# Kernel tuning notes

Hardware: AMD Instinct MI355X
Metric: run time of the kernel (lower is better)

Reference implementation:

```python
import jax, jax.numpy as jnp
import numpy as np

N, M, D = 8192, 8192, 256

def setup_inputs() -> dict:
    key = jax.random.key(0)
    ks = jax.random.split(key, 8)
    s = 1.0 / np.sqrt(D)
    return {
        "x_q": jax.random.normal(ks[0], (N, D), dtype=jnp.float32),
        "x_kv": jax.random.normal(ks[1], (M, D), dtype=jnp.float32),
        "Wq": jax.random.uniform(ks[2], (D, D), minval=-s, maxval=s, dtype=jnp.float32),
        "bq": jax.random.uniform(ks[3], (D,), minval=-s, maxval=s, dtype=jnp.float32),
        "Wk": jax.random.uniform(ks[4], (D, D), minval=-s, maxval=s, dtype=jnp.float32),
        "bk": jax.random.uniform(ks[5], (D,), minval=-s, maxval=s, dtype=jnp.float32),
        "Wv": jax.random.uniform(ks[6], (D, D), minval=-s, maxval=s, dtype=jnp.float32),
        "bv": jax.random.uniform(ks[7], (D,), minval=-s, maxval=s, dtype=jnp.float32),
    }

def reference(x_q, x_kv, Wq, bq, Wk, bk, Wv, bv):
    # Linear layers: y = x @ W^T + b (torch convention: W is [out, in])
    q = x_q @ Wq.T + bq          # [N, D]
    k = x_kv @ Wk.T + bk         # [M, D]
    v = x_kv @ Wv.T + bv         # [M, D]
    scale = jnp.sqrt(jnp.asarray(q.shape[1], q.dtype))
    attn = jnp.einsum('nd,md->nm', q, k) / scale  # [N, M]
    attn = jax.nn.softmax(attn, axis=1)
    return attn @ v              # [N, D]
```

## Files before the change

### kernel.cpp

```cpp
#include <hip/hip_runtime.h>

#define NN 8192
#define MM 8192
#define DD 256
#define NPART 8
#define MPART (MM / NPART)
#define BK 64
#define NT (MPART / BK)

#define SCALE_C 0.0901684403f
#define RAW_THR 127.5f

typedef short bf16x8 __attribute__((ext_vector_type(8)));
typedef float f32x4 __attribute__((ext_vector_type(4)));
typedef float f32x16 __attribute__((ext_vector_type(16)));
typedef unsigned int u32;
typedef u32 u32x2 __attribute__((ext_vector_type(2)));
typedef u32 u32x4 __attribute__((ext_vector_type(4)));

#define GLL16(src, dst) __builtin_amdgcn_global_load_lds( \
    (__attribute__((address_space(1))) void*)(src), \
    (__attribute__((address_space(3))) void*)(dst), 16, 0, 0)

static __device__ __forceinline__ unsigned char f2fp8(float a) {
    u32 r;
    asm("v_cvt_pk_fp8_f32 %0, %1, %1" : "=v"(r) : "v"(a));
    return (unsigned char)(r & 0xFFu);
}

static __device__ __forceinline__ u32 cvtpk(float lo, float hi) {
    u32 r;
    asm("v_cvt_pk_bf16_f32 %0, %1, %2" : "=v"(r) : "v"(lo), "v"(hi));
    return r;
}

static __device__ __forceinline__ float bf2f(short s) {
    return __builtin_bit_cast(float, (u32)((unsigned short)s) << 16);
}

__global__ __launch_bounds__(256, 2) void proj_kernel(
    const float* __restrict__ xq, const float* __restrict__ xkv,
    const float* __restrict__ Wq, const float* __restrict__ bq,
    const float* __restrict__ Wk, const float* __restrict__ bk,
    const float* __restrict__ Wv, const float* __restrict__ bv,
    unsigned char* __restrict__ q8, unsigned char* __restrict__ k8,
    short* __restrict__ vp)
{
    __shared__ short Xs[64][264];
    __shared__ short Ws[64][264];

    const int bid = blockIdx.x;
    const int iskv = bid >> 9;
    const int t = bid & 511;
    const int rt = t >> 2;
    const int ct = t & 3;
    const float* __restrict__ X = iskv ? xkv : xq;
    const float* __restrict__ W1 = iskv ? Wk : Wq;

    const int tid = threadIdx.x;
    const int lane = tid & 63;
    const int wv = tid >> 6;
    const int l15 = lane & 15;
    const int lg = lane >> 4;

    #pragma unroll
    for (int i = 0; i < 16; ++i) {
        int c = i * 256 + tid;
        int row = c >> 6;
        int col4 = (c & 63) << 2;
        f32x4 xv = *reinterpret_cast<const f32x4*>(X + (size_t)(rt * 64 + row) * DD + col4);
        f32x4 wr = *reinterpret_cast<const f32x4*>(W1 + (size_t)(ct * 64 + row) * DD + col4);
        u32x2 xb, wb;
        xb[0] = cvtpk(xv[0], xv[1]); xb[1] = cvtpk(xv[2], xv[3]);
        wb[0] = cvtpk(wr[0], wr[1]); wb[1] = cvtpk(wr[2], wr[3]);
        *reinterpret_cast<u32x2*>(&Xs[row][col4]) = xb;
        *reinterpret_cast<u32x2*>(&Ws[row][col4]) = wb;
    }
    __syncthreads();

    f32x4 acc[4];
    #pragma unroll
    for (int f = 0; f < 4; ++f) acc[f] = f32x4{0.f, 0.f, 0.f, 0.f};

    #pragma unroll
    for (int kk = 0; kk < 8; ++kk) {
        bf16x8 a = *reinterpret_cast<const bf16x8*>(&Xs[wv * 16 + l15][kk * 32 + lg * 8]);
        #pragma unroll
        for (int f = 0; f < 4; ++f) {
            bf16x8 b = *reinterpret_cast<const bf16x8*>(&Ws[f * 16 + l15][kk * 32 + lg * 8]);
            acc[f] = __builtin_amdgcn_mfma_f32_16x16x32_bf16(a, b, acc[f], 0, 0, 0);
        }
    }

    if (!iskv) {
        #pragma unroll
        for (int f = 0; f < 4; ++f) {
            const int o = ct * 64 + f * 16 + l15;
            const float bsv = bq[o];
            #pragma unroll
            for (int r = 0; r < 4; ++r) {
                const int rowg = rt * 64 + wv * 16 + lg * 4 + r;
                q8[(size_t)rowg * DD + o] = f2fp8(acc[f][r] + bsv);
            }
        }
        return;
    }

    #pragma unroll
    for (int f = 0; f < 4; ++f) {
        const int o = ct * 64 + f * 16 + l15;
        const float bsv = bk[o];
        #pragma unroll
        for (int r = 0; r < 4; ++r) {
            const int rowg = rt * 64 + wv * 16 + lg * 4 + r;
            k8[(size_t)(o >> 3) * (MM * 8) + (size_t)rowg * 8 + (o & 7)] = f2fp8(acc[f][r] + bsv);
        }
    }

    __syncthreads();
    #pragma unroll
    for (int i = 0; i < 16; ++i) {
        int c = i * 256 + tid;
        int row = c >> 6;
        int col4 = (c & 63) << 2;
        f32x4 wr = *reinterpret_cast<const f32x4*>(Wv + (size_t)(ct * 64 + row) * DD + col4);
        u32x2 wb;
        wb[0] = cvtpk(wr[0], wr[1]); wb[1] = cvtpk(wr[2], wr[3]);
        *reinterpret_cast<u32x2*>(&Ws[row][col4]) = wb;
    }
    __syncthreads();

    #pragma unroll
    for (int f = 0; f < 4; ++f) acc[f] = f32x4{0.f, 0.f, 0.f, 0.f};
    #pragma unroll
    for (int kk = 0; kk < 8; ++kk) {
        bf16x8 a = *reinterpret_cast<const bf16x8*>(&Xs[wv * 16 + l15][kk * 32 + lg * 8]);
        #pragma unroll
        for (int f = 0; f < 4; ++f) {
            bf16x8 b = *reinterpret_cast<const bf16x8*>(&Ws[f * 16 + l15][kk * 32 + lg * 8]);
            acc[f] = __builtin_amdgcn_mfma_f32_16x16x32_bf16(a, b, acc[f], 0, 0, 0);
        }
    }
    #pragma unroll
    for (int f = 0; f < 4; ++f) {
        const int o = ct * 64 + f * 16 + l15;
        const float bsv = bv[o];
        const int mb = rt * 64 + wv * 16 + lg * 4;
        u32x2 pk;
        pk[0] = cvtpk(acc[f][0] + bsv, acc[f][1] + bsv);
        pk[1] = cvtpk(acc[f][2] + bsv, acc[f][3] + bsv);
        *reinterpret_cast<u32x2*>(&vp[(size_t)(mb >> 6) * 16384 + o * 64 + (mb & 63)]) = pk;
    }
}

__global__ __launch_bounds__(512, 2) void attn_kernel(
    const unsigned char* __restrict__ qg, const unsigned char* __restrict__ kg,
    const short* __restrict__ vp, short* __restrict__ outpB,
    float* __restrict__ statm, float* __restrict__ statl)
{
    extern __shared__ short lds[];
    short* KsBase = lds;
    short* VsBase = lds + 3 * 8192;

    const int bid = blockIdx.x;
    const int p = bid & 7;
    const int qt = bid >> 3;
    const int q0 = qt * 256;
    const int tile0 = p * NT;

    const int tid = threadIdx.x;
    const int lane = tid & 63;
    const int w = tid >> 6;
    const int l31 = lane & 31;
    const int h = lane >> 5;

    long qf8[16];
    {
        const unsigned char* qr = qg + (size_t)(q0 + w * 32 + l31) * DD + h * 8;
        #pragma unroll
        for (int kt = 0; kt < 16; ++kt)
            qf8[kt] = __builtin_bit_cast(long, *reinterpret_cast<const u32x2*>(qr + kt * 16));
    }

    int koff[2], jdstK[2], voff[4], jdstV[4];
    #pragma unroll
    for (int i = 0; i < 2; ++i) {
        const int j = w * 2 + i;
        const int pl = 2 * j + (lane >> 5);
        koff[i] = pl * (MM * 8) + (lane & 31) * 16;
        jdstK[i] = __builtin_amdgcn_readfirstlane(j * 512);
    }
    #pragma unroll
    for (int i = 0; i < 4; ++i) {
        const int j = w * 4 + i;
        const int d = j * 8 + (lane >> 3);
        const int cl = ((lane & 7) - (d & 7)) & 7;
        voff[i] = d * 64 + (cl << 3);
        jdstV[i] = __builtin_amdgcn_readfirstlane(j * 512);
    }

    f32x16 o[8];
    #pragma unroll
    for (int dt = 0; dt < 8; ++dt)
        #pragma unroll
        for (int i = 0; i < 16; ++i) o[dt][i] = 0.f;
    float mrun = -1e30f, lrun = 0.f;
    bf16x8 pb[4];

    #pragma unroll
    for (int i = 0; i < 2; ++i)
        GLL16(kg + (size_t)tile0 * 512 + koff[i], KsBase + jdstK[i]);
    #pragma unroll
    for (int i = 0; i < 4; ++i)
        GLL16(vp + (size_t)tile0 * 16384 + voff[i], VsBase + jdstV[i]);
    #pragma unroll
    for (int i = 0; i < 2; ++i)
        GLL16(kg + (size_t)(tile0 + 1) * 512 + koff[i], KsBase + 8192 + jdstK[i]);
    asm volatile("s_waitcnt vmcnt(6)\n\ts_barrier" ::: "memory");

    {
        const char* kb = (const char*)KsBase;
        #pragma unroll
        for (int i = 0; i < 4; ++i)
            GLL16(vp + (size_t)(tile0 + 1) * 16384 + voff[i], VsBase + 16384 + jdstV[i]);
        #pragma unroll
        for (int i = 0; i < 2; ++i)
            GLL16(kg + (size_t)(tile0 + 2) * 512 + koff[i], KsBase + 2 * 8192 + jdstK[i]);

        f32x16 sL, sH;
        #pragma unroll
        for (int i = 0; i < 16; ++i) { sL[i] = 0.f; sH[i] = 0.f; }
        __builtin_amdgcn_s_setprio(1);
        #pragma unroll
        for (int kt = 0; kt < 16; ++kt) {
            const int gb = (kt * 2 + h) * 512 + l31 * 8;
            long aL = __builtin_bit_cast(long, *reinterpret_cast<const u32x2*>(kb + gb));
            long aH = __builtin_bit_cast(long, *reinterpret_cast<const u32x2*>(kb + gb + 256));
            sL = __builtin_amdgcn_mfma_f32_32x32x16_fp8_fp8(aL, qf8[kt], sL, 0, 0, 0);
            sH = __builtin_amdgcn_mfma_f32_32x32x16_fp8_fp8(aH, qf8[kt], sH, 0, 0, 0);
        }
        __builtin_amdgcn_s_setprio(0);

        float mx;
        {
            float a0 = fmaxf(fmaxf(sL[0], sL[1]), fmaxf(sL[2], sL[3]));
            float a1 = fmaxf(fmaxf(sL[4], sL[5]), fmaxf(sL[6], sL[7]));
            float a2 = fmaxf(fmaxf(sL[8], sL[9]), fmaxf(sL[10], sL[11]));
            float a3 = fmaxf(fmaxf(sL[12], sL[13]), fmaxf(sL[14], sL[15]));
            float b0 = fmaxf(fmaxf(sH[0], sH[1]), fmaxf(sH[2], sH[3]));
            float b1 = fmaxf(fmaxf(sH[4], sH[5]), fmaxf(sH[6], sH[7]));
            float b2 = fmaxf(fmaxf(sH[8], sH[9]), fmaxf(sH[10], sH[11]));
            float b3 = fmaxf(fmaxf(sH[12], sH[13]), fmaxf(sH[14], sH[15]));
            mx = fmaxf(fmaxf(fmaxf(a0, a1), fmaxf(a2, a3)),
                       fmaxf(fmaxf(b0, b1), fmaxf(b2, b3)));
            mx = fmaxf(mx, __shfl_xor(mx, 32));
        }
        mrun = mx;
        const float msc = -mrun * SCALE_C;
        #pragma unroll
        for (int i = 0; i < 16; ++i) {
            sL[i] = __builtin_amdgcn_exp2f(fmaf(sL[i], SCALE_C, msc));
            sH[i] = __builtin_amdgcn_exp2f(fmaf(sH[i], SCALE_C, msc));
        }
        {
            float r0 = ((sL[0] + sL[1]) + (sL[2] + sL[3])) + ((sL[4] + sL[5]) + (sL[6] + sL[7]));
            float r1 = ((sL[8] + sL[9]) + (sL[10] + sL[11])) + ((sL[12] + sL[13]) + (sL[14] + sL[15]));
            float r2 = ((sH[0] + sH[1]) + (sH[2] + sH[3])) + ((sH[4] + sH[5]) + (sH[6] + sH[7]));
            float r3 = ((sH[8] + sH[9]) + (sH[10] + sH[11])) + ((sH[12] + sH[13]) + (sH[14] + sH[15]));
            float rs = (r0 + r1) + (r2 + r3);
            rs += __shfl_xor(rs, 32);
            lrun += rs;
        }
        #pragma unroll
        for (int half = 0; half < 2; ++half) {
            const f32x16& sv = half ? sH : sL;
            #pragma unroll
            for (int g = 0; g < 2; ++g) {
                u32 pa = cvtpk(sv[g * 8 + 0], sv[g * 8 + 1]);
                u32 pbq = cvtpk(sv[g * 8 + 2], sv[g * 8 + 3]);
                u32 pc = cvtpk(sv[g * 8 + 4], sv[g * 8 + 5]);
                u32 pd = cvtpk(sv[g * 8 + 6], sv[g * 8 + 7]);
                const u32 xa = (u32)__shfl_xor((int)pa, 32);
                const u32 xb = (u32)__shfl_xor((int)pbq, 32);
                const u32 xc = (u32)__shfl_xor((int)pc, 32);
                const u32 xd = (u32)__shfl_xor((int)pd, 32);
                u32x4 bb;
                bb[0] = h ? xc : pa;
                bb[1] = h ? xd : pbq;
                bb[2] = h ? pc : xa;
                bb[3] = h ? pd : xb;
                pb[half * 2 + g] = __builtin_bit_cast(bf16x8, bb);
            }
        }
        asm volatile("s_waitcnt vmcnt(6)\n\ts_barrier" ::: "memory");
    }

    int cur = 1;
    #pragma unroll 1
    for (int t = 1; t < NT; ++t) {
        const char* kb = (const char*)(KsBase + cur * 8192);
        const int vprev = (cur == 0) ? 2 : cur - 1;
        const char* vbp = (const char*)(VsBase + vprev * 16384);

        if (t + 1 < NT) {
            const int vw = (cur == 2) ? 0 : cur + 1;
            const size_t tb = (size_t)(tile0 + t + 1) * 16384;
            short* vd = VsBase + vw * 16384;
            #pragma unroll
            for (int i = 0; i < 4; ++i) GLL16(vp + tb + voff[i], vd + jdstV[i]);
        }
        if (t + 2 < NT) {
            const size_t tb = (size_t)(tile0 + t + 2) * 512;
            short* kd = KsBase + vprev * 8192;
            #pragma unroll
            for (int i = 0; i < 2; ++i) GLL16(kg + tb + koff[i], kd + jdstK[i]);
        }

        f32x16 sL, sH;
        #pragma unroll
        for (int i = 0; i < 16; ++i) { sL[i] = 0.f; sH[i] = 0.f; }
        __builtin_amdgcn_s_setprio(1);
        #pragma unroll
        for (int kt = 0; kt < 16; ++kt) {
            const int gb = (kt * 2 + h) * 512 + l31 * 8;
            long aL = __builtin_bit_cast(long, *reinterpret_cast<const u32x2*>(kb + gb));
            long aH = __builtin_bit_cast(long, *reinterpret_cast<const u32x2*>(kb + gb + 256));
            sL = __builtin_amdgcn_mfma_f32_32x32x16_fp8_fp8(aL, qf8[kt], sL, 0, 0, 0);
            sH = __builtin_amdgcn_mfma_f32_32x32x16_fp8_fp8(aH, qf8[kt], sH, 0, 0, 0);
            {
                const int j = 2 * kt;
                const int dt = j & 7, ks = j >> 3;
                const int d = dt * 32 + l31;
                bf16x8 av = *reinterpret_cast<const bf16x8*>(
                    vbp + d * 128 + (((2 * ks + h + (d & 7)) & 7) << 4));
                o[dt] = __builtin_amdgcn_mfma_f32_32x32x16_bf16(av, pb[ks], o[dt], 0, 0, 0);
            }
            {
                const int j = 2 * kt + 1;
                const int dt = j & 7, ks = j >> 3;
                const int d = dt * 32 + l31;
                bf16x8 av = *reinterpret_cast<const bf16x8*>(
                    vbp + d * 128 + (((2 * ks + h + (d & 7)) & 7) << 4));
                o[dt] = __builtin_amdgcn_mfma_f32_32x32x16_bf16(av, pb[ks], o[dt], 0, 0, 0);
            }
        }
        __builtin_amdgcn_s_setprio(0);

        float mx;
        {
            float a0 = fmaxf(fmaxf(sL[0], sL[1]), fmaxf(sL[2], sL[3]));
            float a1 = fmaxf(fmaxf(sL[4], sL[5]), fmaxf(sL[6], sL[7]));
            float a2 = fmaxf(fmaxf(sL[8], sL[9]), fmaxf(sL[10], sL[11]));
            float a3 = fmaxf(fmaxf(sL[12], sL[13]), fmaxf(sL[14], sL[15]));
            float b0 = fmaxf(fmaxf(sH[0], sH[1]), fmaxf(sH[2], sH[3]));
            float b1 = fmaxf(fmaxf(sH[4], sH[5]), fmaxf(sH[6], sH[7]));
            float b2 = fmaxf(fmaxf(sH[8], sH[9]), fmaxf(sH[10], sH[11]));
            float b3 = fmaxf(fmaxf(sH[12], sH[13]), fmaxf(sH[14], sH[15]));
            mx = fmaxf(fmaxf(fmaxf(a0, a1), fmaxf(a2, a3)),
                       fmaxf(fmaxf(b0, b1), fmaxf(b2, b3)));
            mx = fmaxf(mx, __shfl_xor(mx, 32));
        }
        if (__any(mx > mrun + RAW_THR)) {
            const float mn = fmaxf(mrun, mx);
            const float al = __builtin_amdgcn_exp2f((mrun - mn) * SCALE_C);
            mrun = mn;
            lrun *= al;
            #pragma unroll
            for (int dt = 0; dt < 8; ++dt)
                #pragma unroll
                for (int i = 0; i < 16; ++i) o[dt][i] *= al;
        }
        const float msc = -mrun * SCALE_C;
        #pragma unroll
        for (int i = 0; i < 16; ++i) {
            sL[i] = __builtin_amdgcn_exp2f(fmaf(sL[i], SCALE_C, msc));
            sH[i] = __builtin_amdgcn_exp2f(fmaf(sH[i], SCALE_C, msc));
        }
        {
            float r0 = ((sL[0] + sL[1]) + (sL[2] + sL[3])) + ((sL[4] + sL[5]) + (sL[6] + sL[7]));
            float r1 = ((sL[8] + sL[9]) + (sL[10] + sL[11])) + ((sL[12] + sL[13]) + (sL[14] + sL[15]));
            float r2 = ((sH[0] + sH[1]) + (sH[2] + sH[3])) + ((sH[4] + sH[5]) + (sH[6] + sH[7]));
            float r3 = ((sH[8] + sH[9]) + (sH[10] + sH[11])) + ((sH[12] + sH[13]) + (sH[14] + sH[15]));
            float rs = (r0 + r1) + (r2 + r3);
            rs += __shfl_xor(rs, 32);
            lrun += rs;
        }
        #pragma unroll
        for (int half = 0; half < 2; ++half) {
            const f32x16& sv = half ? sH : sL;
            #pragma unroll
            for (int g = 0; g < 2; ++g) {
                u32 pa = cvtpk(sv[g * 8 + 0], sv[g * 8 + 1]);
                u32 pbq = cvtpk(sv[g * 8 + 2], sv[g * 8 + 3]);
                u32 pc = cvtpk(sv[g * 8 + 4], sv[g * 8 + 5]);
                u32 pd = cvtpk(sv[g * 8 + 6], sv[g * 8 + 7]);
                const u32 xa = (u32)__shfl_xor((int)pa, 32);
                const u32 xb = (u32)__shfl_xor((int)pbq, 32);
                const u32 xc = (u32)__shfl_xor((int)pc, 32);
                const u32 xd = (u32)__shfl_xor((int)pd, 32);
                u32x4 bb;
                bb[0] = h ? xc : pa;
                bb[1] = h ? xd : pbq;
                bb[2] = h ? pc : xa;
                bb[3] = h ? pd : xb;
                pb[half * 2 + g] = __builtin_bit_cast(bf16x8, bb);
            }
        }

        if (t + 2 < NT) {
            asm volatile("s_waitcnt vmcnt(6)\n\ts_barrier" ::: "memory");
        } else if (t + 1 < NT) {
            asm volatile("s_waitcnt vmcnt(4)\n\ts_barrier" ::: "memory");
        } else {
            asm volatile("s_waitcnt vmcnt(0)\n\ts_barrier" ::: "memory");
        }
        cur = (cur == 2) ? 0 : cur + 1;
    }

    {
        const char* vb = (const char*)(VsBase + ((NT - 1) % 3) * 16384);
        __builtin_amdgcn_s_setprio(1);
        #pragma unroll
        for (int dt = 0; dt < 8; ++dt) {
            const int d = dt * 32 + l31;
            const char* rbase = vb + d * 128;
            const int rot = d & 7;
            bf16x8 a0 = *reinterpret_cast<const bf16x8*>(rbase + (((0 + h + rot) & 7) << 4));
            bf16x8 a1 = *reinterpret_cast<const bf16x8*>(rbase + (((2 + h + rot) & 7) << 4));
            bf16x8 a2 = *reinterpret_cast<const bf16x8*>(rbase + (((4 + h + rot) & 7) << 4));
            bf16x8 a3 = *reinterpret_cast<const bf16x8*>(rbase + (((6 + h + rot) & 7) << 4));
            o[dt] = __builtin_amdgcn_mfma_f32_32x32x16_bf16(a0, pb[0], o[dt], 0, 0, 0);
            o[dt] = __builtin_amdgcn_mfma_f32_32x32x16_bf16(a1, pb[1], o[dt], 0, 0, 0);
            o[dt] = __builtin_amdgcn_mfma_f32_32x32x16_bf16(a2, pb[2], o[dt], 0, 0, 0);
            o[dt] = __builtin_amdgcn_mfma_f32_32x32x16_bf16(a3, pb[3], o[dt], 0, 0, 0);
        }
        __builtin_amdgcn_s_setprio(0);
    }

    const int qc = q0 + w * 32 + l31;
    #pragma unroll
    for (int dt = 0; dt < 8; ++dt) {
        #pragma unroll
        for (int i = 0; i < 16; i += 2) {
            const u32 two = cvtpk(o[dt][i], o[dt][i + 1]);
            const int dg = dt * 32 + (i & 3) + 8 * (i >> 2) + 4 * h;
            outpB[((size_t)p * DD + dg) * NN + qc] = (short)(two & 0xFFFFu);
            outpB[((size_t)p * DD + dg + 1) * NN + qc] = (short)(two >> 16);
        }
    }
    if (h == 0) {
        statm[(size_t)p * NN + qc] = mrun;
        statl[(size_t)p * NN + qc] = lrun;
    }
}

__global__ __launch_bounds__(1024) void combine_kernel(
    const short* __restrict__ outpB, const float* __restrict__ statm,
    const float* __restrict__ statl, float* __restrict__ out)
{
    __shared__ float Wn[NPART][64];
    __shared__ float Ot[64][DD + 2];

    const int q0 = blockIdx.x * 64;
    const int tid = threadIdx.x;

    if (tid < 64) {
        const int q = q0 + tid;
        float mv[NPART], lv[NPART];
        float mM = -1e30f;
        #pragma unroll
        for (int p = 0; p < NPART; ++p) {
            mv[p] = statm[(size_t)p * NN + q];
            lv[p] = statl[(size_t)p * NN + q];
            mM = fmaxf(mM, mv[p]);
        }
        float L = 0.f;
        float wg[NPART];
        #pragma unroll
        for (int p = 0; p < NPART; ++p) {
            wg[p] = exp2f((mv[p] - mM) * SCALE_C);
            L += wg[p] * lv[p];
        }
        const float inv = 1.0f / L;
        #pragma unroll
        for (int p = 0; p < NPART; ++p) Wn[p][tid] = wg[p] * inv;
    }
    __syncthreads();

    {
        const int pr = tid & 31;
        const int d0 = tid >> 5;
        const float w0 = Wn[0][pr * 2], w0b = Wn[0][pr * 2 + 1];
        (void)w0; (void)w0b;
        #pragma unroll 2
        for (int d = d0; d < DD; d += 32) {
            float a0 = 0.f, a1 = 0.f;
            #pragma unroll
            for (int p = 0; p < NPART; ++p) {
                const u32 two = *reinterpret_cast<const u32*>(
                    &outpB[((size_t)p * DD + d) * NN + q0 + pr * 2]);
                a0 += Wn[p][pr * 2] * __builtin_bit_cast(float, two << 16);
                a1 += Wn[p][pr * 2 + 1] * __builtin_bit_cast(float, two & 0xFFFF0000u);
            }
            Ot[pr * 2][d] = a0;
            Ot[pr * 2 + 1][d] = a1;
        }
    }
    __syncthreads();

    {
        const int qq = tid >> 4;
        const int c = tid & 15;
        #pragma unroll
        for (int j = 0; j < 4; ++j) {
            const int d = c * 16 + j * 4;
            *reinterpret_cast<f32x4*>(&out[(size_t)(q0 + qq) * DD + d]) =
                *reinterpret_cast<const f32x4*>(&Ot[qq][d]);
        }
    }
}

extern "C" void kernel_launch(void* const* d_in, const int* in_sizes, int n_in,
                              void* d_out, int out_size, void* d_ws, size_t ws_size,
                              hipStream_t stream) {
    const float* xq  = (const float*)d_in[0];
    const float* xkv = (const float*)d_in[1];
    const float* Wq  = (const float*)d_in[2];
    const float* bq  = (const float*)d_in[3];
    const float* Wk  = (const float*)d_in[4];
    const float* bk  = (const float*)d_in[5];
    const float* Wv  = (const float*)d_in[6];
    const float* bv  = (const float*)d_in[7];
    float* out = (float*)d_out;

    char* ws = (char*)d_ws;
    unsigned char* qb8 = (unsigned char*)(ws);
    unsigned char* kb8 = (unsigned char*)(ws + ((size_t)4 << 20));
    short* vpb = (short*)(ws + ((size_t)8 << 20));
    short* outpB = (short*)(ws + ((size_t)12 << 20));
    float* sm = (float*)(ws + ((size_t)12 << 20) + (size_t)NPART * NN * DD * 2);
    float* sl = sm + (size_t)NPART * NN;

    hipFuncSetAttribute(reinterpret_cast<const void*>(attn_kernel),
                        hipFuncAttributeMaxDynamicSharedMemorySize, 147456);

    proj_kernel<<<1024, 256, 0, stream>>>(xq, xkv, Wq, bq, Wk, bk, Wv, bv, qb8, kb8, vpb);
    attn_kernel<<<256, 512, 147456, stream>>>(qb8, kb8, vpb, outpB, sm, sl);
    combine_kernel<<<NN / 64, 1024, 0, stream>>>(outpB, sm, sl, out);
}
```

Measured before the change: 97.27 us.

## Restructure projection kernel so each block covers all output columns with double-buffered weights

The projection kernel now launches one block per 64-row tile of x, 256 blocks instead of 1024. Each block loads and converts its X tile once, then loops over 4 (Q) or 8 (K and V) output-column passes. The next weight tile is prefetched into a second LDS buffer while MFMAs run on the current one. This removes the repeated X loads and conversions done by the four column-tile blocks, at the cost of fewer blocks (one per CU at most, with roughly 100KB of dynamic LDS) and more serial work per block. Unused helper code is also removed.

```diff
diff --git a/kernel.cpp b/kernel.cpp
--- a/kernel.cpp
+++ b/kernel.cpp
@@ -34,11 +34,7 @@
     return r;
 }
 
-static __device__ __forceinline__ float bf2f(short s) {
-    return __builtin_bit_cast(float, (u32)((unsigned short)s) << 16);
-}
-
-__global__ __launch_bounds__(256, 2) void proj_kernel(
+__global__ __launch_bounds__(256, 1) void proj_kernel(
     const float* __restrict__ xq, const float* __restrict__ xkv,
     const float* __restrict__ Wq, const float* __restrict__ bq,
     const float* __restrict__ Wk, const float* __restrict__ bk,
@@ -46,16 +42,16 @@
     unsigned char* __restrict__ q8, unsigned char* __restrict__ k8,
     short* __restrict__ vp)
 {
-    __shared__ short Xs[64][264];
-    __shared__ short Ws[64][264];
+    extern __shared__ short plds[];
+    short (*Xs)[264] = (short(*)[264])plds;
+    short (*Ws)[64][264] = (short(*)[64][264])(plds + 16896);
 
     const int bid = blockIdx.x;
-    const int iskv = bid >> 9;
-    const int t = bid & 511;
-    const int rt = t >> 2;
-    const int ct = t & 3;
+    const int iskv = bid >> 7;
+    const int rt = bid & 127;
     const float* __restrict__ X = iskv ? xkv : xq;
-    const float* __restrict__ W1 = iskv ? Wk : Wq;
+    const float* __restrict__ W0 = iskv ? Wk : Wq;
+    const int npass = iskv ? 8 : 4;
 
     const int tid = threadIdx.x;
     const int lane = tid & 63;
@@ -69,87 +65,83 @@
         int row = c >> 6;
         int col4 = (c & 63) << 2;
         f32x4 xv = *reinterpret_cast<const f32x4*>(X + (size_t)(rt * 64 + row) * DD + col4);
-        f32x4 wr = *reinterpret_cast<const f32x4*>(W1 + (size_t)(ct * 64 + row) * DD + col4);
+        f32x4 wr = *reinterpret_cast<const f32x4*>(W0 + (size_t)row * DD + col4);
         u32x2 xb, wb;
         xb[0] = cvtpk(xv[0], xv[1]); xb[1] = cvtpk(xv[2], xv[3]);
         wb[0] = cvtpk(wr[0], wr[1]); wb[1] = cvtpk(wr[2], wr[3]);
         *reinterpret_cast<u32x2*>(&Xs[row][col4]) = xb;
-        *reinterpret_cast<u32x2*>(&Ws[row][col4]) = wb;
+        *reinterpret_cast<u32x2*>(&Ws[0][row][col4]) = wb;
     }
     __syncthreads();
 
-    f32x4 acc[4];
-    #pragma unroll
-    for (int f = 0; f < 4; ++f) acc[f] = f32x4{0.f, 0.f, 0.f, 0.f};
-
-    #pragma unroll
-    for (int kk = 0; kk < 8; ++kk) {
-        bf16x8 a = *reinterpret_cast<const bf16x8*>(&Xs[wv * 16 + l15][kk * 32 + lg * 8]);
-        #pragma unroll
-        for (int f = 0; f < 4; ++f) {
-            bf16x8 b = *reinterpret_cast<const bf16x8*>(&Ws[f * 16 + l15][kk * 32 + lg * 8]);
-            acc[f] = __builtin_amdgcn_mfma_f32_16x16x32_bf16(a, b, acc[f], 0, 0, 0);
-        }
-    }
-
-    if (!iskv) {
-        #pragma unroll
-        for (int f = 0; f < 4; ++f) {
-            const int o = ct * 64 + f * 16 + l15;
-            const float bsv = bq[o];
-            #pragma unroll
-            for (int r = 0; r < 4; ++r) {
-                const int rowg = rt * 64 + wv * 16 + lg * 4 + r;
-                q8[(size_t)rowg * DD + o] = f2fp8(acc[f][r] + bsv);
-            }
-        }
-        return;
-    }
-
-    #pragma unroll
-    for (int f = 0; f < 4; ++f) {
-        const int o = ct * 64 + f * 16 + l15;
-        const float bsv = bk[o];
-        #pragma unroll
-        for (int r = 0; r < 4; ++r) {
-            const int rowg = rt * 64 + wv * 16 + lg * 4 + r;
-            k8[(size_t)(o >> 3) * (MM * 8) + (size_t)rowg * 8 + (o & 7)] = f2fp8(acc[f][r] + bsv);
-        }
-    }
-
-    __syncthreads();
-    #pragma unroll
-    for (int i = 0; i < 16; ++i) {
-        int c = i * 256 + tid;
-        int row = c >> 6;
-        int col4 = (c & 63) << 2;
-        f32x4 wr = *reinterpret_cast<const f32x4*>(Wv + (size_t)(ct * 64 + row) * DD + col4);
-        u32x2 wb;
-        wb[0] = cvtpk(wr[0], wr[1]); wb[1] = cvtpk(wr[2], wr[3]);
-        *reinterpret_cast<u32x2*>(&Ws[row][col4]) = wb;
-    }
-    __syncthreads();
-
-    #pragma unroll
-    for (int f = 0; f < 4; ++f) acc[f] = f32x4{0.f, 0.f, 0.f, 0.f};
-    #pragma unroll
-    for (int kk = 0; kk < 8; ++kk) {
-        bf16x8 a = *reinterpret_cast<const bf16x8*>(&Xs[wv * 16 + l15][kk * 32 + lg * 8]);
-        #pragma unroll
-        for (int f = 0; f < 4; ++f) {
-            bf16x8 b = *reinterpret_cast<const bf16x8*>(&Ws[f * 16 + l15][kk * 32 + lg * 8]);
-            acc[f] = __builtin_amdgcn_mfma_f32_16x16x32_bf16(a, b, acc[f], 0, 0, 0);
-        }
-    }
-    #pragma unroll
-    for (int f = 0; f < 4; ++f) {
-        const int o = ct * 64 + f * 16 + l15;
-        const float bsv = bv[o];
-        const int mb = rt * 64 + wv * 16 + lg * 4;
-        u32x2 pk;
-        pk[0] = cvtpk(acc[f][0] + bsv, acc[f][1] + bsv);
-        pk[1] = cvtpk(acc[f][2] + bsv, acc[f][3] + bsv);
-        *reinterpret_cast<u32x2*>(&vp[(size_t)(mb >> 6) * 16384 + o * 64 + (mb & 63)]) = pk;
+    #pragma unroll 1
+    for (int pass = 0; pass < npass; ++pass) {
+        const int cur = pass & 1;
+        if (pass + 1 < npass) {
+            const int np = pass + 1;
+            const float* __restrict__ Wn = iskv ? ((np < 4) ? Wk : Wv) : Wq;
+            const int nct = np & 3;
+            #pragma unroll
+            for (int i = 0; i < 16; ++i) {
+                int c = i * 256 + tid;
+                int row = c >> 6;
+                int col4 = (c & 63) << 2;
+                f32x4 wr = *reinterpret_cast<const f32x4*>(Wn + (size_t)(nct * 64 + row) * DD + col4);
+                u32x2 wb;
+                wb[0] = cvtpk(wr[0], wr[1]); wb[1] = cvtpk(wr[2], wr[3]);
+                *reinterpret_cast<u32x2*>(&Ws[cur ^ 1][row][col4]) = wb;
+            }
+        }
+
+        f32x4 acc[4];
+        #pragma unroll
+        for (int f = 0; f < 4; ++f) acc[f] = f32x4{0.f, 0.f, 0.f, 0.f};
+        #pragma unroll
+        for (int kk = 0; kk < 8; ++kk) {
+            bf16x8 a = *reinterpret_cast<const bf16x8*>(&Xs[wv * 16 + l15][kk * 32 + lg * 8]);
+            #pragma unroll
+            for (int f = 0; f < 4; ++f) {
+                bf16x8 b = *reinterpret_cast<const bf16x8*>(&Ws[cur][f * 16 + l15][kk * 32 + lg * 8]);
+                acc[f] = __builtin_amdgcn_mfma_f32_16x16x32_bf16(a, b, acc[f], 0, 0, 0);
+            }
+        }
+
+        const int ct = pass & 3;
+        if (!iskv) {
+            #pragma unroll
+            for (int f = 0; f < 4; ++f) {
+                const int o = ct * 64 + f * 16 + l15;
+                const float bsv = bq[o];
+                #pragma unroll
+                for (int r = 0; r < 4; ++r) {
+                    const int rowg = rt * 64 + wv * 16 + lg * 4 + r;
+                    q8[(size_t)rowg * DD + o] = f2fp8(acc[f][r] + bsv);
+                }
+            }
+        } else if (pass < 4) {
+            #pragma unroll
+            for (int f = 0; f < 4; ++f) {
+                const int o = ct * 64 + f * 16 + l15;
+                const float bsv = bk[o];
+                #pragma unroll
+                for (int r = 0; r < 4; ++r) {
+                    const int rowg = rt * 64 + wv * 16 + lg * 4 + r;
+                    k8[(size_t)(o >> 3) * (MM * 8) + (size_t)rowg * 8 + (o & 7)] = f2fp8(acc[f][r] + bsv);
+                }
+            }
+        } else {
+            #pragma unroll
+            for (int f = 0; f < 4; ++f) {
+                const int o = ct * 64 + f * 16 + l15;
+                const float bsv = bv[o];
+                const int mb = rt * 64 + wv * 16 + lg * 4;
+                u32x2 pk;
+                pk[0] = cvtpk(acc[f][0] + bsv, acc[f][1] + bsv);
+                pk[1] = cvtpk(acc[f][2] + bsv, acc[f][3] + bsv);
+                *reinterpret_cast<u32x2*>(&vp[(size_t)(mb >> 6) * 16384 + o * 64 + (mb & 63)]) = pk;
+            }
+        }
+        __syncthreads();
     }
 }
 
@@ -490,8 +482,6 @@
     {
         const int pr = tid & 31;
         const int d0 = tid >> 5;
-        const float w0 = Wn[0][pr * 2], w0b = Wn[0][pr * 2 + 1];
-        (void)w0; (void)w0b;
         #pragma unroll 2
         for (int d = d0; d < DD; d += 32) {
             float a0 = 0.f, a1 = 0.f;
@@ -541,10 +531,12 @@
     float* sm = (float*)(ws + ((size_t)12 << 20) + (size_t)NPART * NN * DD * 2);
     float* sl = sm + (size_t)NPART * NN;
 
+    hipFuncSetAttribute(reinterpret_cast<const void*>(proj_kernel),
+                        hipFuncAttributeMaxDynamicSharedMemorySize, 101376);
     hipFuncSetAttribute(reinterpret_cast<const void*>(attn_kernel),
                         hipFuncAttributeMaxDynamicSharedMemorySize, 147456);
 
-    proj_kernel<<<1024, 256, 0, stream>>>(xq, xkv, Wq, bq, Wk, bk, Wv, bv, qb8, kb8, vpb);
+    proj_kernel<<<256, 256, 101376, stream>>>(xq, xkv, Wq, bq, Wk, bk, Wv, bv, qb8, kb8, vpb);
     attn_kernel<<<256, 512, 147456, stream>>>(qb8, kb8, vpb, outpB, sm, sl);
     combine_kernel<<<NN / 64, 1024, 0, stream>>>(outpB, sm, sl, out);
 }
```

New measurement: 99.09 us. About the same (+1.9%).
